# Performance work log

Hardware: AMD Instinct MI355X
Metric: run time of the kernel (lower is better)

The kernel has to match this reference:

```python
import jax, jax.numpy as jnp
from jax import lax
import numpy as np

DIM = 96
D_STATE = 16
D_CONV = 4
EXPAND = 2
D_INNER = EXPAND * DIM


def _layernorm(x, g, b, eps=1e-5):
    mu = jnp.mean(x, axis=-1, keepdims=True)
    var = jnp.var(x, axis=-1, keepdims=True)
    return (x - mu) * lax.rsqrt(var + eps) * g + b


def _pssm(x, Wp, cw, cb, A, Dp, Wo):
    # x: (B, L, C)
    Bn, L, _ = x.shape
    xp = x @ Wp                                  # (B, L, 3*d_inner)
    x_conv, delta, BC = jnp.split(xp, 3, axis=-1)
    # causal depthwise conv1d (torch pads d_conv-1 both sides then slices [:L] == left pad)
    xc = lax.conv_general_dilated(
        jnp.transpose(x_conv, (0, 2, 1)), cw, (1,), [(D_CONV - 1, 0)],
        dimension_numbers=('NCH', 'OIH', 'NCH'), feature_group_count=D_INNER)
    xc = jnp.transpose(xc, (0, 2, 1)) + cb       # (B, L, d_inner)
    delta = jax.nn.sigmoid(delta)                # (B, L, d_inner)
    Bm = BC[..., :D_STATE]                       # (B, L, N) input gate
    Cm = BC[..., D_STATE:2 * D_STATE]            # (B, L, N) output gate
    # literal einsum 'bnl,ij->bnil' sums A over j -> row-sums vector
    Asum = jnp.sum(A, axis=1)                    # (N,)
    a = jnp.exp(delta[:, :, None, :] * Asum[None, None, :, None])   # (B,L,N,d)
    bu = (delta * xc)[:, :, None, :] * Bm[..., None]                 # (B,L,N,d)

    def scan_dir(a_, b_):
        def step(h, ab):
            at, bt = ab
            h = at * h + bt
            return h, h
        _, hs = lax.scan(step, jnp.zeros_like(a_[:, 0]),
                         (jnp.moveaxis(a_, 1, 0), jnp.moveaxis(b_, 1, 0)))
        return jnp.moveaxis(hs, 0, 1)            # (B, L, N, d)

    h = scan_dir(a, bu) + scan_dir(a[:, ::-1], bu[:, ::-1])[:, ::-1]
    y = jnp.einsum('blnd,bln->bld', h, Cm) + Dp * xc
    return y @ Wo                                # (B, L, C)


def _forward(x, norm_g, norm_b,
             Wp1, cw1, cb1, A1, Dp1, Wo1, lng1, lnb1,
             Wp2, cw2, cb2, A2, Dp2, Wo2, lng2, lnb2,
             Wf, bf, W1, b1, W2, b2):
    Bn, H, W_, C = x.shape
    res = x
    xn = _layernorm(x, norm_g, norm_b)
    xs = xn.reshape(Bn, H * W_, C)
    f1 = _layernorm(_pssm(xs, Wp1, cw1, cb1, A1, Dp1, Wo1), lng1, lnb1).reshape(Bn, H, W_, C)
    f2 = _layernorm(_pssm(xs, Wp2, cw2, cb2, A2, Dp2, Wo2), lng2, lnb2).reshape(Bn, H, W_, C)
    EPS = 1e-12
    n1 = f1 / jnp.maximum(jnp.linalg.norm(f1, axis=-1, keepdims=True), EPS)
    n2 = f2 / jnp.maximum(jnp.linalg.norm(f2, axis=-1, keepdims=True), EPS)
    sim = jnp.sum(n1 * n2, axis=-1, keepdims=True)          # (B,H,W,1)
    fused = sim * f1 + (1.0 - sim) * f2
    cat = jnp.concatenate([f1, fused], axis=-1)             # (B,H,W,2C)
    fc = lax.conv_general_dilated(cat, Wf, (1, 1), 'SAME',
                                  dimension_numbers=('NHWC', 'HWIO', 'NHWC')) + bf
    fc = jax.nn.gelu(fc, approximate=False)
    y = jax.nn.gelu(fc @ W1 + b1, approximate=False) @ W2 + b2
    return y + res


def setup_inputs() -> dict:
    key = jax.random.key(0)
    ks = jax.random.split(key, 32)
    B, H, W, C = 2, 64, 64, DIM

    def n(k, shape, s=1.0):
        return jax.random.normal(k, shape, dtype=jnp.float32) * s

    inp = {}
    inp['x'] = n(ks[0], (B, H, W, C))
    inp['norm_g'] = jnp.ones((C,), jnp.float32)
    inp['norm_b'] = jnp.zeros((C,), jnp.float32)
    for i, off in enumerate([1, 10]):
        p = str(i + 1)
        inp['Wp' + p] = n(ks[off], (C, 3 * D_INNER), 0.02)
        inp['cw' + p] = n(ks[off + 1], (D_INNER, 1, D_CONV), 0.1)
        inp['cb' + p] = jnp.zeros((D_INNER,), jnp.float32)
        # negative A row-sums keep exp(delta*Asum) < 1 -> stable scan over L=4096
        inp['A' + p] = -jnp.abs(n(ks[off + 2], (D_STATE, D_STATE))) * 0.1
        inp['Dp' + p] = n(ks[off + 3], (D_INNER,), 0.1)
        inp['Wo' + p] = n(ks[off + 4], (D_INNER, C), 0.02)
        inp['lng' + p] = jnp.ones((C,), jnp.float32)
        inp['lnb' + p] = jnp.zeros((C,), jnp.float32)
    inp['Wf'] = n(ks[20], (3, 3, 2 * C, C), 0.02)
    inp['bf'] = jnp.zeros((C,), jnp.float32)
    inp['W1'] = n(ks[21], (C, 4 * C), 0.02)
    inp['b1'] = jnp.zeros((4 * C,), jnp.float32)
    inp['W2'] = n(ks[22], (4 * C, C), 0.02)
    inp['b2'] = jnp.zeros((C,), jnp.float32)
    return inp


def reference(x, norm_g, norm_b,
              Wp1, cw1, cb1, A1, Dp1, Wo1, lng1, lnb1,
              Wp2, cw2, cb2, A2, Dp2, Wo2, lng2, lnb2,
              Wf, bf, W1, b1, W2, b2):
    return _forward(x, norm_g, norm_b,
                    Wp1, cw1, cb1, A1, Dp1, Wo1, lng1, lnb1,
                    Wp2, cw2, cb2, A2, Dp2, Wo2, lng2, lnb2,
                    Wf, bf, W1, b1, W2, b2)
```

## Files before the change

kernel.cpp:

```cpp
#include <hip/hip_runtime.h>
#include <hip/hip_bf16.h>
#include <math.h>

#define L_SEQ 4096
#define CDIM 96
#define DIN 192
#define NST 16
#define NCHUNK 64
#define CHLEN 64
#define MROWS 8192
#define XPW2 960
#define SCAN_GRID 3072

typedef __attribute__((ext_vector_type(8))) short bf16x8;
typedef __attribute__((ext_vector_type(4))) float f32x4;
typedef __attribute__((ext_vector_type(4))) short s16x4;
typedef __attribute__((ext_vector_type(4))) unsigned short u16x4;

__device__ __forceinline__ float gelu_exact(float x) {
    return 0.5f * x * (1.0f + erff(x * 0.70710678118654752f));
}

__device__ __forceinline__ float fast_exp2(float x) {
#if __has_builtin(__builtin_amdgcn_exp2f)
    return __builtin_amdgcn_exp2f(x);
#else
    return exp2f(x);
#endif
}

__device__ __forceinline__ float b2f(unsigned short u) {
    return __uint_as_float((unsigned int)u << 16);
}

__device__ __forceinline__ float rowsum16(float s) {
    s += __int_as_float(__builtin_amdgcn_update_dpp(0, __float_as_int(s), 0x128, 0xF, 0xF, true));
    s += __int_as_float(__builtin_amdgcn_update_dpp(0, __float_as_int(s), 0x124, 0xF, 0xF, true));
    s += __int_as_float(__builtin_amdgcn_update_dpp(0, __float_as_int(s), 0x122, 0xF, 0xF, true));
    s += __int_as_float(__builtin_amdgcn_update_dpp(0, __float_as_int(s), 0x121, 0xF, 0xF, true));
    return s;
}

__device__ __forceinline__ unsigned short f2bf_bits(float f) {
    __hip_bfloat16 h = __float2bfloat16(f);
    return *reinterpret_cast<unsigned short*>(&h);
}

#define CVT_BLOCKS 1440
__global__ __launch_bounds__(256) void prep_kernel(
    const float* __restrict__ Wp0, const float* __restrict__ Wp1,
    const float* __restrict__ Wo0, const float* __restrict__ Wo1,
    const float* __restrict__ Wf, const float* __restrict__ W1, const float* __restrict__ W2,
    __hip_bfloat16* __restrict__ wpT, __hip_bfloat16* __restrict__ wo0T,
    __hip_bfloat16* __restrict__ wo1T, __hip_bfloat16* __restrict__ wfT,
    __hip_bfloat16* __restrict__ w1T, __hip_bfloat16* __restrict__ w2T,
    const float* __restrict__ x, const float* __restrict__ g, const float* __restrict__ b,
    __hip_bfloat16* __restrict__ xn) {
    if (blockIdx.x >= CVT_BLOCKS) {
        int wave = threadIdx.x >> 6;
        int lane = threadIdx.x & 63;
        int row = (blockIdx.x - CVT_BLOCKS) * 4 + wave;
        if (row >= MROWS) return;
        const float* p = x + (size_t)row * CDIM;
        float x0 = p[lane];
        float x1 = (lane < 32) ? p[64 + lane] : 0.f;
        float s = x0 + x1, sq = x0 * x0 + x1 * x1;
#pragma unroll
        for (int o = 32; o >= 1; o >>= 1) { s += __shfl_xor(s, o); sq += __shfl_xor(sq, o); }
        float mean = s * (1.f / 96.f);
        float var = sq * (1.f / 96.f) - mean * mean;
        float w = rsqrtf(var + 1e-5f);
        __hip_bfloat16* q = xn + (size_t)row * CDIM;
        q[lane] = __float2bfloat16((x0 - mean) * w * g[lane] + b[lane]);
        if (lane < 32) q[64 + lane] = __float2bfloat16((x1 - mean) * w * g[64 + lane] + b[64 + lane]);
        return;
    }
    int i = blockIdx.x * 256 + threadIdx.x;
    const int S_WPALL = XPW2 * 96;
    const int S_WO = 96 * 192;
    const int S_WF = 96 * 1728;
    const int S_W1 = 384 * 96;
    const int S_W2 = 96 * 384;
    if (i < S_WPALL) {
        int j = i / 96, r = i % 96;
        int br = j / 480, cc = j % 480;
        const float* W = br ? Wp1 : Wp0;
        wpT[i] = __float2bfloat16(cc < 416 ? W[r * 576 + cc] : 0.f);
        return;
    }
    i -= S_WPALL;
    if (i < S_WO) { int c = i / 192, r = i % 192; wo0T[i] = __float2bfloat16(Wo0[r * 96 + c]); return; }
    i -= S_WO;
    if (i < S_WO) { int c = i / 192, r = i % 192; wo1T[i] = __float2bfloat16(Wo1[r * 96 + c]); return; }
    i -= S_WO;
    if (i < S_WF) { int c = i / 1728, k = i % 1728; wfT[i] = __float2bfloat16(Wf[k * 96 + c]); return; }
    i -= S_WF;
    if (i < S_W1) { int c = i / 96, r = i % 96; w1T[i] = __float2bfloat16(W1[r * 384 + c]); return; }
    i -= S_W1;
    if (i < S_W2) { int c = i / 384, r = i % 384; w2T[i] = __float2bfloat16(W2[r * 96 + c]); return; }
}

template <int MI, int NI, int WR, int WC, int K, int KS, int EPI, typename CT>
__global__ __launch_bounds__(WR * WC * KS * 64) void gemm_direct(
    const __hip_bfloat16* __restrict__ A, int lda,
    const __hip_bfloat16* __restrict__ BT,
    CT* __restrict__ C, int ldc, int N,
    const float* __restrict__ bias, const float* __restrict__ res) {
    __shared__ float part[KS > 1 ? (WR * MI * 16) * (WC * NI * 16) : 1];
    int tid = threadIdx.x;
    int lane = tid & 63, wid = tid >> 6;
    int wk = wid / (WR * WC);
    int wrem = wid % (WR * WC);
    int wm = wrem % WR, wn = wrem / WR;
    int m0 = blockIdx.y * (WR * MI * 16) + wm * MI * 16;
    int n0 = blockIdx.x * (WC * NI * 16) + wn * NI * 16;
    int lr = lane & 15, kh = (lane >> 4) * 8;
    constexpr int KC = K / KS;
    f32x4 acc[MI][NI] = {};
    const __hip_bfloat16* Ap = A + (size_t)(m0 + lr) * lda + kh + wk * KC;
    const __hip_bfloat16* Bp = BT + (size_t)(n0 + lr) * K + kh + wk * KC;
#pragma unroll
    for (int k0 = 0; k0 < KC; k0 += 32) {
        bf16x8 af[MI], bf[NI];
#pragma unroll
        for (int i = 0; i < MI; ++i)
            af[i] = *reinterpret_cast<const bf16x8*>(Ap + (size_t)i * 16 * lda + k0);
#pragma unroll
        for (int j = 0; j < NI; ++j)
            bf[j] = *reinterpret_cast<const bf16x8*>(Bp + (size_t)j * 16 * K + k0);
#pragma unroll
        for (int i = 0; i < MI; ++i)
#pragma unroll
            for (int j = 0; j < NI; ++j)
                acc[i][j] = __builtin_amdgcn_mfma_f32_16x16x32_bf16(af[i], bf[j], acc[i][j], 0, 0, 0);
    }
    int cr = (lane >> 4) << 2;
    if (KS > 1) {
        constexpr int BN = WC * NI * 16;
        if (wk == 1) {
#pragma unroll
            for (int i = 0; i < MI; ++i)
#pragma unroll
                for (int j = 0; j < NI; ++j)
#pragma unroll
                    for (int q = 0; q < 4; ++q)
                        part[(wm * MI * 16 + i * 16 + cr + q) * BN + wn * NI * 16 + j * 16 + lr] =
                            acc[i][j][q];
        }
        __syncthreads();
        if (wk != 0) return;
#pragma unroll
        for (int i = 0; i < MI; ++i)
#pragma unroll
            for (int j = 0; j < NI; ++j)
#pragma unroll
                for (int q = 0; q < 4; ++q)
                    acc[i][j][q] +=
                        part[(wm * MI * 16 + i * 16 + cr + q) * BN + wn * NI * 16 + j * 16 + lr];
    }
#pragma unroll
    for (int i = 0; i < MI; ++i) {
        int row = m0 + i * 16 + cr;
#pragma unroll
        for (int j = 0; j < NI; ++j) {
            int col = n0 + j * 16 + lr;
            if (col < N) {
#pragma unroll
                for (int q = 0; q < 4; ++q) {
                    float v = acc[i][j][q];
                    if (EPI == 1) v = gelu_exact(v + bias[col]);
                    else if (EPI == 2) v = v + bias[col] + res[(size_t)(row + q) * ldc + col];
                    C[(size_t)(row + q) * ldc + col] = (CT)v;
                }
            }
        }
    }
}

__global__ __launch_bounds__(256) void gemm_wo_ln_fuse(
    const __hip_bfloat16* __restrict__ A,
    const __hip_bfloat16* __restrict__ BT0, const __hip_bfloat16* __restrict__ BT1,
    const float* __restrict__ g0, const float* __restrict__ b0,
    const float* __restrict__ g1, const float* __restrict__ b1,
    __hip_bfloat16* __restrict__ cat) {
    int tid = threadIdx.x;
    int lane = tid & 63, wid = tid >> 6;
    int wm = wid & 1, wn = wid >> 1;
    int m0 = blockIdx.x * 32 + wm * 16;
    int n0 = wn * 48;
    int lr = lane & 15, kh = (lane >> 4) * 8;
    f32x4 acc0[3] = {}, acc1[3] = {};
    const __hip_bfloat16* A0 = A + (size_t)(m0 + lr) * 192 + kh;
    const __hip_bfloat16* A1 = A + (size_t)(MROWS + m0 + lr) * 192 + kh;
    const __hip_bfloat16* Bp0 = BT0 + (size_t)(n0 + lr) * 192 + kh;
    const __hip_bfloat16* Bp1 = BT1 + (size_t)(n0 + lr) * 192 + kh;
#pragma unroll
    for (int k0 = 0; k0 < 192; k0 += 32) {
        bf16x8 af0 = *reinterpret_cast<const bf16x8*>(A0 + k0);
        bf16x8 af1 = *reinterpret_cast<const bf16x8*>(A1 + k0);
#pragma unroll
        for (int j = 0; j < 3; ++j) {
            bf16x8 b0v = *reinterpret_cast<const bf16x8*>(Bp0 + (size_t)j * 16 * 192 + k0);
            bf16x8 b1v = *reinterpret_cast<const bf16x8*>(Bp1 + (size_t)j * 16 * 192 + k0);
            acc0[j] = __builtin_amdgcn_mfma_f32_16x16x32_bf16(af0, b0v, acc0[j], 0, 0, 0);
            acc1[j] = __builtin_amdgcn_mfma_f32_16x16x32_bf16(af1, b1v, acc1[j], 0, 0, 0);
        }
    }
    __shared__ float ct0[32][100], ct1[32][100];
    int cr = (lane >> 4) << 2;
#pragma unroll
    for (int j = 0; j < 3; ++j)
#pragma unroll
        for (int q = 0; q < 4; ++q) {
            ct0[wm * 16 + cr + q][n0 + j * 16 + lr] = acc0[j][q];
            ct1[wm * 16 + cr + q][n0 + j * 16 + lr] = acc1[j][q];
        }
    __syncthreads();
#pragma unroll
    for (int rr = 0; rr < 8; ++rr) {
        int row = wid * 8 + rr;
        float a0 = ct0[row][lane];
        float a1 = (lane < 32) ? ct0[row][64 + lane] : 0.f;
        float c0 = ct1[row][lane];
        float c1 = (lane < 32) ? ct1[row][64 + lane] : 0.f;
        float s0 = a0 + a1, q0 = a0 * a0 + a1 * a1;
        float s1 = c0 + c1, q1 = c0 * c0 + c1 * c1;
#pragma unroll
        for (int o = 32; o >= 1; o >>= 1) {
            s0 += __shfl_xor(s0, o); q0 += __shfl_xor(q0, o);
            s1 += __shfl_xor(s1, o); q1 += __shfl_xor(q1, o);
        }
        float mu0 = s0 * (1.f / 96.f), w0 = rsqrtf(q0 * (1.f / 96.f) - mu0 * mu0 + 1e-5f);
        float mu1 = s1 * (1.f / 96.f), w1 = rsqrtf(q1 * (1.f / 96.f) - mu1 * mu1 + 1e-5f);
        float f1a = (a0 - mu0) * w0 * g0[lane] + b0[lane];
        float f2a = (c0 - mu1) * w1 * g1[lane] + b1[lane];
        float f1b = 0.f, f2b = 0.f;
        if (lane < 32) {
            f1b = (a1 - mu0) * w0 * g0[64 + lane] + b0[64 + lane];
            f2b = (c1 - mu1) * w1 * g1[64 + lane] + b1[64 + lane];
        }
        float s11 = f1a * f1a + f1b * f1b;
        float s22 = f2a * f2a + f2b * f2b;
        float s12 = f1a * f2a + f1b * f2b;
#pragma unroll
        for (int o = 32; o >= 1; o >>= 1) {
            s11 += __shfl_xor(s11, o);
            s22 += __shfl_xor(s22, o);
            s12 += __shfl_xor(s12, o);
        }
        float nr1 = fmaxf(sqrtf(s11), 1e-12f);
        float nr2 = fmaxf(sqrtf(s22), 1e-12f);
        float sim = s12 / (nr1 * nr2);
        size_t grow = (size_t)blockIdx.x * 32 + row;
        __hip_bfloat16* q = cat + grow * 192;
        q[lane] = __float2bfloat16(f1a);
        q[96 + lane] = __float2bfloat16(sim * f1a + (1.f - sim) * f2a);
        if (lane < 32) {
            q[64 + lane] = __float2bfloat16(f1b);
            q[96 + 64 + lane] = __float2bfloat16(sim * f1b + (1.f - sim) * f2b);
        }
    }
}

__global__ __launch_bounds__(512) void conv3x3_direct(const __hip_bfloat16* __restrict__ cat,
                                                      const __hip_bfloat16* __restrict__ WfT,
                                                      const float* __restrict__ bfv,
                                                      __hip_bfloat16* __restrict__ out) {
    __shared__ float part[32][96];
    int tid = threadIdx.x;
    int lane = tid & 63, wid = tid >> 6;
    int wm = wid & 1, wn = (wid >> 1) & 1, wk = wid >> 2;
    int m0 = blockIdx.x * 32 + wm * 16;
    int n0 = wn * 48;
    int lr = lane & 15, kh = (lane >> 4) * 8;
    int m = m0 + lr;
    int bb = m >> 12, l = m & 4095, yy = l >> 6, xx = l & 63;
    f32x4 acc[3] = {};
    const __hip_bfloat16* Bp = WfT + (size_t)(n0 + lr) * 1728 + kh;
#pragma unroll
    for (int tap = 0; tap < 9; ++tap) {
        if ((tap & 1) != wk) continue;
        int ky = tap / 3, kx = tap % 3;
        int iy = yy + ky - 1, ix = xx + kx - 1;
        bool ok = ((unsigned)iy < 64u) && ((unsigned)ix < 64u);
        const __hip_bfloat16* Ap = cat + ((size_t)bb * 4096 + (size_t)(iy * 64 + ix)) * 192 + kh;
        int kbase = tap * 192;
#pragma unroll
        for (int kc = 0; kc < 192; kc += 32) {
            bf16x8 af = {};
            if (ok) af = *reinterpret_cast<const bf16x8*>(Ap + kc);
#pragma unroll
            for (int j = 0; j < 3; ++j) {
                bf16x8 bf = *reinterpret_cast<const bf16x8*>(Bp + (size_t)j * 16 * 1728 + kbase + kc);
                acc[j] = __builtin_amdgcn_mfma_f32_16x16x32_bf16(af, bf, acc[j], 0, 0, 0);
            }
        }
    }
    int cr = (lane >> 4) << 2;
    if (wk == 1) {
#pragma unroll
        for (int j = 0; j < 3; ++j)
#pragma unroll
            for (int q = 0; q < 4; ++q)
                part[wm * 16 + cr + q][n0 + j * 16 + lr] = acc[j][q];
    }
    __syncthreads();
    if (wk != 0) return;
    int crow = m0 + cr;
#pragma unroll
    for (int j = 0; j < 3; ++j) {
        int ccol = n0 + j * 16 + lr;
#pragma unroll
        for (int q = 0; q < 4; ++q) {
            float v = acc[j][q] + part[wm * 16 + cr + q][ccol];
            v = gelu_exact(v + bfv[ccol]);
            out[(size_t)(crow + q) * 96 + ccol] = __float2bfloat16(v);
        }
    }
}

__global__ __launch_bounds__(256) void scan_pass1f(
    const __hip_bfloat16* __restrict__ xpw,
    const float* __restrict__ cw0, const float* __restrict__ cw1,
    const float* __restrict__ cb0, const float* __restrict__ cb1,
    const float* __restrict__ A0, const float* __restrict__ A1,
    float* __restrict__ Pc, float* __restrict__ Hf, float* __restrict__ Gb) {
    __shared__ unsigned short rawxu[67][16];
    __shared__ float2 sdx[CHLEN][16];
    __shared__ float sb[CHLEN][16];
    __shared__ float asumv[16];
    int bid = (blockIdx.x & 7) * (SCAN_GRID / 8) + (blockIdx.x >> 3);
    int dg = bid % 12;
    int c = (bid / 12) % NCHUNK;
    int b = (bid / (12 * NCHUNK)) & 1;
    int p = bid / (12 * NCHUNK * 2);
    const float* cw = p ? cw1 : cw0;
    const float* cbp = p ? cb1 : cb0;
    const float* Am = p ? A1 : A0;
    int tid = threadIdx.x;
    if (tid < 16) {
        const float4* Ap4 = (const float4*)(Am + tid * 16);
        float4 a0 = Ap4[0], a1 = Ap4[1], a2 = Ap4[2], a3 = Ap4[3];
        float s = (a0.x + a0.y + a0.z + a0.w) + (a1.x + a1.y + a1.z + a1.w) +
                  (a2.x + a2.y + a2.z + a2.w) + (a3.x + a3.y + a3.z + a3.w);
        asumv[tid] = s * 1.44269504f;
    }
    const unsigned short* xu = (const unsigned short*)xpw;
    int xb = p * 480;
    int t0 = c * CHLEN;
    int r = tid >> 2, q = (tid & 3) * 4;
    size_t grow = (size_t)b * L_SEQ + t0 + r;
    const unsigned short* rowp = xu + grow * XPW2 + xb;
    *(u16x4*)&rawxu[r + 3][q] = *(const u16x4*)(rowp + dg * 16 + q);
    u16x4 dvu = *(const u16x4*)(rowp + 192 + dg * 16 + q);
    u16x4 bvu = *(const u16x4*)(rowp + 384 + q);
    float4 bf4 = {b2f(bvu.x), b2f(bvu.y), b2f(bvu.z), b2f(bvu.w)};
    *(float4*)&sb[r][q] = bf4;
    if (tid < 12) {
        int rr = tid >> 2, qq = (tid & 3) * 4;
        int src = t0 - 3 + rr;
        u16x4 v = {0, 0, 0, 0};
        if (src >= 0)
            v = *(const u16x4*)(xu + ((size_t)b * L_SEQ + src) * XPW2 + xb + dg * 16 + qq);
        *(u16x4*)&rawxu[rr][qq] = v;
    }
    __syncthreads();
    float dd[4] = {b2f(dvu.x), b2f(dvu.y), b2f(dvu.z), b2f(dvu.w)};
#pragma unroll
    for (int i = 0; i < 4; ++i) {
        int d = dg * 16 + q + i;
        float4 w = *(const float4*)(cw + (size_t)d * 4);
        float xc = cbp[d] + w.w * b2f(rawxu[r + 3][q + i]) + w.z * b2f(rawxu[r + 2][q + i]) +
                   w.y * b2f(rawxu[r + 1][q + i]) + w.x * b2f(rawxu[r][q + i]);
        float ds = 1.f / (1.f + __expf(-dd[i]));
        sdx[r][q + i] = make_float2(ds, ds * xc);
    }
    __syncthreads();
    int n = tid & 15, drow = tid >> 4;
    float asum2 = asumv[n];
    float h = 0.f, gb = 0.f, Q = 1.f;
#pragma unroll 4
    for (int t = 0; t < CHLEN; ++t) {
        float2 dx = sdx[t][drow];
        float bm = sb[t][n];
        float a = fast_exp2(dx.x * asum2);
        float bu = dx.y * bm;
        h = a * h + bu;
        gb += Q * bu;
        Q *= a;
    }
    size_t cidx = ((((size_t)p * 2 + b) * NST + n) * DIN + dg * 16 + drow) * NCHUNK + c;
    Pc[cidx] = Q;
    Hf[cidx] = h;
    Gb[cidx] = gb;
}

__global__ __launch_bounds__(256) void scan_pass2(const float* __restrict__ Pc,
                                                  const float* __restrict__ Hf,
                                                  const float* __restrict__ Gb,
                                                  float* __restrict__ Hinf,
                                                  float* __restrict__ Hinb) {
    int t = blockIdx.x * 256 + threadIdx.x;
    if (t >= 2 * 2 * NST * DIN) return;
    size_t base = (size_t)t * NCHUNK;
    {
        float4 P4[16], H4[16];
        const float4* Pp = (const float4*)(Pc + base);
        const float4* Hp = (const float4*)(Hf + base);
#pragma unroll
        for (int i = 0; i < 16; ++i) { P4[i] = Pp[i]; H4[i] = Hp[i]; }
        float hin = 0.f;
        float4* Op = (float4*)(Hinf + base);
#pragma unroll
        for (int i = 0; i < 16; ++i) {
            float4 o;
            o.x = hin; hin = H4[i].x + P4[i].x * hin;
            o.y = hin; hin = H4[i].y + P4[i].y * hin;
            o.z = hin; hin = H4[i].z + P4[i].z * hin;
            o.w = hin; hin = H4[i].w + P4[i].w * hin;
            Op[i] = o;
        }
    }
    {
        float4 P4[16], G4[16];
        const float4* Pp = (const float4*)(Pc + base);
        const float4* Gp = (const float4*)(Gb + base);
#pragma unroll
        for (int i = 0; i < 16; ++i) { P4[i] = Pp[i]; G4[i] = Gp[i]; }
        float gin = 0.f;
        float4* Op = (float4*)(Hinb + base);
#pragma unroll
        for (int i = 15; i >= 0; --i) {
            float4 o;
            o.w = gin; gin = G4[i].w + P4[i].w * gin;
            o.z = gin; gin = G4[i].z + P4[i].z * gin;
            o.y = gin; gin = G4[i].y + P4[i].y * gin;
            o.x = gin; gin = G4[i].x + P4[i].x * gin;
            Op[i] = o;
        }
    }
}

__global__ __launch_bounds__(512) void scan_pass3f(
    const __hip_bfloat16* __restrict__ xpw,
    const float* __restrict__ cw0, const float* __restrict__ cw1,
    const float* __restrict__ cb0, const float* __restrict__ cb1,
    const float* __restrict__ A0, const float* __restrict__ A1,
    const float* __restrict__ Hinf, const float* __restrict__ Hinb,
    const float* __restrict__ Dp0, const float* __restrict__ Dp1,
    __hip_bfloat16* __restrict__ y) {
    __shared__ unsigned short rawxu[67][16];
    __shared__ float2 sdx[CHLEN][16];
    __shared__ float2 sbc[CHLEN][16];
    __shared__ unsigned short sxcu[CHLEN][16];
    __shared__ float ysf[CHLEN][16], ysb[CHLEN][16];
    __shared__ float asumv[16];
    int bid = (blockIdx.x & 7) * (SCAN_GRID / 8) + (blockIdx.x >> 3);
    int dg = bid % 12;
    int c = (bid / 12) % NCHUNK;
    int b = (bid / (12 * NCHUNK)) & 1;
    int p = bid / (12 * NCHUNK * 2);
    const float* cw = p ? cw1 : cw0;
    const float* cbp = p ? cb1 : cb0;
    const float* Am = p ? A1 : A0;
    const float* Dp = p ? Dp1 : Dp0;
    int tid = threadIdx.x;
    if (tid < 16) {
        const float4* Ap4 = (const float4*)(Am + tid * 16);
        float4 a0 = Ap4[0], a1 = Ap4[1], a2 = Ap4[2], a3 = Ap4[3];
        float s = (a0.x + a0.y + a0.z + a0.w) + (a1.x + a1.y + a1.z + a1.w) +
                  (a2.x + a2.y + a2.z + a2.w) + (a3.x + a3.y + a3.z + a3.w);
        asumv[tid] = s * 1.44269504f;
    }
    const unsigned short* xu = (const unsigned short*)xpw;
    int xb = p * 480;
    int t0 = c * CHLEN;
    int r = tid >> 2, q = (tid & 3) * 4;
    u16x4 dvu = {0, 0, 0, 0};
    if (tid < 256) {
        size_t grow = (size_t)b * L_SEQ + t0 + r;
        const unsigned short* rowp = xu + grow * XPW2 + xb;
        *(u16x4*)&rawxu[r + 3][q] = *(const u16x4*)(rowp + dg * 16 + q);
        dvu = *(const u16x4*)(rowp + 192 + dg * 16 + q);
        u16x4 bvu = *(const u16x4*)(rowp + 384 + q);
        u16x4 cvu = *(const u16x4*)(rowp + 400 + q);
        sbc[r][q + 0] = make_float2(b2f(bvu.x), b2f(cvu.x));
        sbc[r][q + 1] = make_float2(b2f(bvu.y), b2f(cvu.y));
        sbc[r][q + 2] = make_float2(b2f(bvu.z), b2f(cvu.z));
        sbc[r][q + 3] = make_float2(b2f(bvu.w), b2f(cvu.w));
        if (tid < 12) {
            int rr = tid >> 2, qq = (tid & 3) * 4;
            int src = t0 - 3 + rr;
            u16x4 v = {0, 0, 0, 0};
            if (src >= 0)
                v = *(const u16x4*)(xu + ((size_t)b * L_SEQ + src) * XPW2 + xb + dg * 16 + qq);
            *(u16x4*)&rawxu[rr][qq] = v;
        }
    }
    __syncthreads();
    if (tid < 256) {
        float dd[4] = {b2f(dvu.x), b2f(dvu.y), b2f(dvu.z), b2f(dvu.w)};
#pragma unroll
        for (int i = 0; i < 4; ++i) {
            int d = dg * 16 + q + i;
            float4 w = *(const float4*)(cw + (size_t)d * 4);
            float xc = cbp[d] + w.w * b2f(rawxu[r + 3][q + i]) + w.z * b2f(rawxu[r + 2][q + i]) +
                       w.y * b2f(rawxu[r + 1][q + i]) + w.x * b2f(rawxu[r][q + i]);
            float ds = 1.f / (1.f + __expf(-dd[i]));
            sdx[r][q + i] = make_float2(ds, ds * xc);
            sxcu[r][q + i] = f2bf_bits(xc);
        }
    }
    __syncthreads();
    int lane = tid & 63, wave = tid >> 6;
    int dir = wave >> 2;
    int wl = wave & 3;
    int n = lane & 15;
    int dloc = wl * 4 + (lane >> 4);
    int d = dg * 16 + dloc;
    float asum2 = asumv[n];
    size_t cidx = ((((size_t)p * 2 + b) * NST + n) * DIN + d) * NCHUNK + c;
    if (dir == 0) {
        float h = Hinf[cidx];
#pragma unroll 4
        for (int t = 0; t < CHLEN; ++t) {
            float2 dx = sdx[t][dloc];
            float2 bc = sbc[t][n];
            float a = fast_exp2(dx.x * asum2);
            h = a * h + dx.y * bc.x;
            float pf = rowsum16(bc.y * h);
            if (n == 0) ysf[t][dloc] = pf;
        }
    } else {
        float gv = Hinb[cidx];
#pragma unroll 4
        for (int t = CHLEN - 1; t >= 0; --t) {
            float2 dx = sdx[t][dloc];
            float2 bc = sbc[t][n];
            float a = fast_exp2(dx.x * asum2);
            gv = a * gv + dx.y * bc.x;
            float pb = rowsum16(bc.y * gv);
            if (n == 0) ysb[t][dloc] = pb;
        }
    }
    __syncthreads();
    if (tid < 256) {
        int tl = tid >> 2, qq = (tid & 3) * 4;
        int d2 = dg * 16 + qq;
        float4 Dv = *(const float4*)(Dp + d2);
        float vs[4];
#pragma unroll
        for (int i = 0; i < 4; ++i)
            vs[i] = ysf[tl][qq + i] + ysb[tl][qq + i] +
                    ((const float*)&Dv)[i] * b2f(sxcu[tl][qq + i]);
        s16x4 pk = {(short)f2bf_bits(vs[0]), (short)f2bf_bits(vs[1]),
                    (short)f2bf_bits(vs[2]), (short)f2bf_bits(vs[3])};
        size_t row = (size_t)b * L_SEQ + t0 + tl;
        *(s16x4*)((unsigned short*)y + ((size_t)p * MROWS + row) * DIN + d2) = pk;
    }
}

extern "C" void kernel_launch(void* const* d_in, const int* in_sizes, int n_in,
                              void* d_out, int out_size, void* d_ws, size_t ws_size,
                              hipStream_t stream) {
    const float* x = (const float*)d_in[0];
    const float* norm_g = (const float*)d_in[1];
    const float* norm_b = (const float*)d_in[2];
    const float* Wp[2] = {(const float*)d_in[3], (const float*)d_in[11]};
    const float* cw[2] = {(const float*)d_in[4], (const float*)d_in[12]};
    const float* cb[2] = {(const float*)d_in[5], (const float*)d_in[13]};
    const float* Ab[2] = {(const float*)d_in[6], (const float*)d_in[14]};
    const float* Dpb[2] = {(const float*)d_in[7], (const float*)d_in[15]};
    const float* Wo[2] = {(const float*)d_in[8], (const float*)d_in[16]};
    const float* lng[2] = {(const float*)d_in[9], (const float*)d_in[17]};
    const float* lnb[2] = {(const float*)d_in[10], (const float*)d_in[18]};
    const float* Wf = (const float*)d_in[19];
    const float* bfv = (const float*)d_in[20];
    const float* W1 = (const float*)d_in[21];
    const float* b1 = (const float*)d_in[22];
    const float* W2 = (const float*)d_in[23];
    const float* b2 = (const float*)d_in[24];
    float* out = (float*)d_out;

    char* base = (char*)d_ws;
    size_t off = 0;
    auto alloc = [&](size_t bytes) { void* p = base + off; off += (bytes + 255) & ~(size_t)255; return p; };
    __hip_bfloat16* xpw = (__hip_bfloat16*)alloc((size_t)MROWS * XPW2 * 2);
    const size_t csz = (size_t)2 * 2 * NST * DIN * NCHUNK;
    float* Pc = (float*)alloc(csz * 4);
    float* Hfc = (float*)alloc(csz * 4);
    float* Gbc = (float*)alloc(csz * 4);
    float* Hinf = (float*)alloc(csz * 4);
    float* Hinb = (float*)alloc(csz * 4);
    __hip_bfloat16* xn_bf = (__hip_bfloat16*)alloc((size_t)MROWS * 96 * 2);
    __hip_bfloat16* yb_bf = (__hip_bfloat16*)alloc((size_t)2 * MROWS * DIN * 2);
    __hip_bfloat16* cat_bf = (__hip_bfloat16*)alloc((size_t)MROWS * DIN * 2);
    __hip_bfloat16* fc_bf = (__hip_bfloat16*)alloc((size_t)MROWS * 96 * 2);
    __hip_bfloat16* h1_bf = (__hip_bfloat16*)alloc((size_t)MROWS * 384 * 2);
    __hip_bfloat16* wpT = (__hip_bfloat16*)alloc((size_t)XPW2 * 96 * 2);
    __hip_bfloat16* woT[2] = {(__hip_bfloat16*)alloc(96 * 192 * 2),
                              (__hip_bfloat16*)alloc(96 * 192 * 2)};
    __hip_bfloat16* wfT = (__hip_bfloat16*)alloc(96 * 1728 * 2);
    __hip_bfloat16* w1T = (__hip_bfloat16*)alloc(384 * 96 * 2);
    __hip_bfloat16* w2T = (__hip_bfloat16*)alloc(96 * 384 * 2);
    (void)ws_size; (void)in_sizes; (void)n_in; (void)out_size;

    prep_kernel<<<dim3(CVT_BLOCKS + 2048), dim3(256), 0, stream>>>(
        Wp[0], Wp[1], Wo[0], Wo[1], Wf, W1, W2,
        wpT, woT[0], woT[1], wfT, w1T, w2T, x, norm_g, norm_b, xn_bf);
    gemm_direct<2, 3, 2, 2, 96, 1, 0, __hip_bfloat16><<<dim3(10, 128), dim3(256), 0, stream>>>(
        xn_bf, 96, wpT, xpw, XPW2, XPW2, nullptr, nullptr);
    scan_pass1f<<<dim3(SCAN_GRID), dim3(256), 0, stream>>>(
        xpw, cw[0], cw[1], cb[0], cb[1], Ab[0], Ab[1], Pc, Hfc, Gbc);
    scan_pass2<<<dim3(48), dim3(256), 0, stream>>>(Pc, Hfc, Gbc, Hinf, Hinb);
    scan_pass3f<<<dim3(SCAN_GRID), dim3(512), 0, stream>>>(
        xpw, cw[0], cw[1], cb[0], cb[1], Ab[0], Ab[1], Hinf, Hinb, Dpb[0], Dpb[1], yb_bf);
    gemm_wo_ln_fuse<<<dim3(256), dim3(256), 0, stream>>>(
        yb_bf, woT[0], woT[1], lng[0], lnb[0], lng[1], lnb[1], cat_bf);
    conv3x3_direct<<<dim3(256), dim3(512), 0, stream>>>(cat_bf, wfT, bfv, fc_bf);
    gemm_direct<2, 3, 2, 2, 96, 1, 1, __hip_bfloat16><<<dim3(4, 128), dim3(256), 0, stream>>>(
        fc_bf, 96, w1T, h1_bf, 384, 384, b1, nullptr);
    gemm_direct<1, 3, 2, 2, 384, 2, 2, float><<<dim3(1, 256), dim3(512), 0, stream>>>(
        h1_bf, 384, w2T, out, 96, 96, b2, x);
}
```

Measured before the change: 155.5 us.

## Split chunk scan pass1 into separate forward and backward waves

Launches scan_pass1f with 512 threads. Half the waves compute the forward chunk state h and the other half run a reverse recurrence that gives the backward carry G and the decay product Q. Previously each thread carried all three values in one serial loop. The dependency chain per thread gets shorter and parallelism doubles, at the cost of computing exp twice and leaving half the threads idle during the load phase. The rowsum16 DPP reductions are also rewritten as inline asm v_add_f32_dpp instructions.

```diff
diff --git a/kernel.cpp b/kernel.cpp
--- a/kernel.cpp
+++ b/kernel.cpp
@@ -34,10 +34,10 @@
 }
 
 __device__ __forceinline__ float rowsum16(float s) {
-    s += __int_as_float(__builtin_amdgcn_update_dpp(0, __float_as_int(s), 0x128, 0xF, 0xF, true));
-    s += __int_as_float(__builtin_amdgcn_update_dpp(0, __float_as_int(s), 0x124, 0xF, 0xF, true));
-    s += __int_as_float(__builtin_amdgcn_update_dpp(0, __float_as_int(s), 0x122, 0xF, 0xF, true));
-    s += __int_as_float(__builtin_amdgcn_update_dpp(0, __float_as_int(s), 0x121, 0xF, 0xF, true));
+    asm("v_add_f32_dpp %0, %0, %0 row_ror:8 row_mask:0xf bank_mask:0xf" : "+v"(s));
+    asm("v_add_f32_dpp %0, %0, %0 row_ror:4 row_mask:0xf bank_mask:0xf" : "+v"(s));
+    asm("v_add_f32_dpp %0, %0, %0 row_ror:2 row_mask:0xf bank_mask:0xf" : "+v"(s));
+    asm("v_add_f32_dpp %0, %0, %0 row_ror:1 row_mask:0xf bank_mask:0xf" : "+v"(s));
     return s;
 }
 
@@ -319,7 +319,7 @@
     }
 }
 
-__global__ __launch_bounds__(256) void scan_pass1f(
+__global__ __launch_bounds__(512) void scan_pass1f(
     const __hip_bfloat16* __restrict__ xpw,
     const float* __restrict__ cw0, const float* __restrict__ cw1,
     const float* __restrict__ cb0, const float* __restrict__ cb1,
@@ -349,50 +349,67 @@
     int xb = p * 480;
     int t0 = c * CHLEN;
     int r = tid >> 2, q = (tid & 3) * 4;
-    size_t grow = (size_t)b * L_SEQ + t0 + r;
-    const unsigned short* rowp = xu + grow * XPW2 + xb;
-    *(u16x4*)&rawxu[r + 3][q] = *(const u16x4*)(rowp + dg * 16 + q);
-    u16x4 dvu = *(const u16x4*)(rowp + 192 + dg * 16 + q);
-    u16x4 bvu = *(const u16x4*)(rowp + 384 + q);
-    float4 bf4 = {b2f(bvu.x), b2f(bvu.y), b2f(bvu.z), b2f(bvu.w)};
-    *(float4*)&sb[r][q] = bf4;
-    if (tid < 12) {
-        int rr = tid >> 2, qq = (tid & 3) * 4;
-        int src = t0 - 3 + rr;
-        u16x4 v = {0, 0, 0, 0};
-        if (src >= 0)
-            v = *(const u16x4*)(xu + ((size_t)b * L_SEQ + src) * XPW2 + xb + dg * 16 + qq);
-        *(u16x4*)&rawxu[rr][qq] = v;
+    u16x4 dvu = {0, 0, 0, 0};
+    if (tid < 256) {
+        size_t grow = (size_t)b * L_SEQ + t0 + r;
+        const unsigned short* rowp = xu + grow * XPW2 + xb;
+        *(u16x4*)&rawxu[r + 3][q] = *(const u16x4*)(rowp + dg * 16 + q);
+        dvu = *(const u16x4*)(rowp + 192 + dg * 16 + q);
+        u16x4 bvu = *(const u16x4*)(rowp + 384 + q);
+        float4 bf4 = {b2f(bvu.x), b2f(bvu.y), b2f(bvu.z), b2f(bvu.w)};
+        *(float4*)&sb[r][q] = bf4;
+        if (tid < 12) {
+            int rr = tid >> 2, qq = (tid & 3) * 4;
+            int src = t0 - 3 + rr;
+            u16x4 v = {0, 0, 0, 0};
+            if (src >= 0)
+                v = *(const u16x4*)(xu + ((size_t)b * L_SEQ + src) * XPW2 + xb + dg * 16 + qq);
+            *(u16x4*)&rawxu[rr][qq] = v;
+        }
     }
     __syncthreads();
-    float dd[4] = {b2f(dvu.x), b2f(dvu.y), b2f(dvu.z), b2f(dvu.w)};
-#pragma unroll
-    for (int i = 0; i < 4; ++i) {
-        int d = dg * 16 + q + i;
-        float4 w = *(const float4*)(cw + (size_t)d * 4);
-        float xc = cbp[d] + w.w * b2f(rawxu[r + 3][q + i]) + w.z * b2f(rawxu[r + 2][q + i]) +
-                   w.y * b2f(rawxu[r + 1][q + i]) + w.x * b2f(rawxu[r][q + i]);
-        float ds = 1.f / (1.f + __expf(-dd[i]));
-        sdx[r][q + i] = make_float2(ds, ds * xc);
+    if (tid < 256) {
+        float dd[4] = {b2f(dvu.x), b2f(dvu.y), b2f(dvu.z), b2f(dvu.w)};
+#pragma unroll
+        for (int i = 0; i < 4; ++i) {
+            int d = dg * 16 + q + i;
+            float4 w = *(const float4*)(cw + (size_t)d * 4);
+            float xc = cbp[d] + w.w * b2f(rawxu[r + 3][q + i]) + w.z * b2f(rawxu[r + 2][q + i]) +
+                       w.y * b2f(rawxu[r + 1][q + i]) + w.x * b2f(rawxu[r][q + i]);
+            float ds = 1.f / (1.f + __expf(-dd[i]));
+            sdx[r][q + i] = make_float2(ds, ds * xc);
+        }
     }
     __syncthreads();
-    int n = tid & 15, drow = tid >> 4;
+    int lane = tid & 63, wave = tid >> 6;
+    int dir = wave >> 2, wl = wave & 3;
+    int n = lane & 15;
+    int drow = wl * 4 + (lane >> 4);
     float asum2 = asumv[n];
-    float h = 0.f, gb = 0.f, Q = 1.f;
+    size_t cidx = ((((size_t)p * 2 + b) * NST + n) * DIN + dg * 16 + drow) * NCHUNK + c;
+    if (dir == 0) {
+        float h = 0.f;
 #pragma unroll 4
-    for (int t = 0; t < CHLEN; ++t) {
-        float2 dx = sdx[t][drow];
-        float bm = sb[t][n];
-        float a = fast_exp2(dx.x * asum2);
-        float bu = dx.y * bm;
-        h = a * h + bu;
-        gb += Q * bu;
-        Q *= a;
-    }
-    size_t cidx = ((((size_t)p * 2 + b) * NST + n) * DIN + dg * 16 + drow) * NCHUNK + c;
-    Pc[cidx] = Q;
-    Hf[cidx] = h;
-    Gb[cidx] = gb;
+        for (int t = 0; t < CHLEN; ++t) {
+            float2 dx = sdx[t][drow];
+            float bm = sb[t][n];
+            float a = fast_exp2(dx.x * asum2);
+            h = a * h + dx.y * bm;
+        }
+        Hf[cidx] = h;
+    } else {
+        float G = 0.f, Q = 1.f;
+#pragma unroll 4
+        for (int t = CHLEN - 1; t >= 0; --t) {
+            float2 dx = sdx[t][drow];
+            float bm = sb[t][n];
+            float a = fast_exp2(dx.x * asum2);
+            G = a * G + dx.y * bm;
+            Q *= a;
+        }
+        Gb[cidx] = G;
+        Pc[cidx] = Q;
+    }
 }
 
 __global__ __launch_bounds__(256) void scan_pass2(const float* __restrict__ Pc,
@@ -610,7 +627,7 @@
         wpT, woT[0], woT[1], wfT, w1T, w2T, x, norm_g, norm_b, xn_bf);
     gemm_direct<2, 3, 2, 2, 96, 1, 0, __hip_bfloat16><<<dim3(10, 128), dim3(256), 0, stream>>>(
         xn_bf, 96, wpT, xpw, XPW2, XPW2, nullptr, nullptr);
-    scan_pass1f<<<dim3(SCAN_GRID), dim3(256), 0, stream>>>(
+    scan_pass1f<<<dim3(SCAN_GRID), dim3(512), 0, stream>>>(
         xpw, cw[0], cw[1], cb[0], cb[1], Ab[0], Ab[1], Pc, Hfc, Gbc);
     scan_pass2<<<dim3(48), dim3(256), 0, stream>>>(Pc, Hfc, Gbc, Hinf, Hinb);
     scan_pass3f<<<dim3(SCAN_GRID), dim3(512), 0, stream>>>(
```

Measured after the change: 157.5 us. No clear change (+1.3%).
